# Kernel tuning notes

Measured on AMD Instinct MI355X. Metric: run time of the kernel, lower is better.

The kernel has to match this reference:

```python
import jax, jax.numpy as jnp
import numpy as np

K = 32  # knn neighborhood size (hard-coded in get_graph_feature)
EPS_BN = 1e-5


def _bn(x, g, b):
    # batch-norm (training-mode batch stats) over all axes except the last (channel) axis
    axes = tuple(range(x.ndim - 1))
    m = jnp.mean(x, axis=axes, keepdims=True)
    v = jnp.var(x, axis=axes, keepdims=True)
    return (x - m) * jax.lax.rsqrt(v + EPS_BN) * g + b


def _knn_idx(xt, k):
    # xt: [B, N, C] -> indices of k nearest points [B, N, k] (torch topk on -||xi-xj||^2)
    xx = jnp.sum(xt * xt, axis=-1)                       # [B, N]
    inner = jnp.einsum('bnc,bmc->bnm', xt, xt)           # [B, N, N]
    neg_d2 = -(xx[:, :, None] - 2.0 * inner + xx[:, None, :])
    _, idx = jax.lax.top_k(neg_d2, k)
    return idx


def _graph_feature(x, k=K):
    # x: [B, C, N] -> feature [B, N, k, 2C] matching torch cat((neighbors, center))
    xt = jnp.transpose(x, (0, 2, 1))                     # [B, N, C]
    idx = _knn_idx(xt, k)                                # [B, N, k]
    gathered = jax.vmap(lambda a, i: a[i])(xt, idx)      # [B, N, k, C]
    center = jnp.broadcast_to(xt[:, :, None, :], gathered.shape)
    return jnp.concatenate([gathered, center], axis=-1)


def _dgcnn(x, w1, w2, w3, w4, w5, g1, g2, g3, g4, g5, b1, b2, b3, b4, b5):
    # x: [B, 3, N] -> embeddings [B, emb, N]
    feat = _graph_feature(x)                                         # [B, N, K, 6]
    h = jax.nn.relu(_bn(jnp.einsum('bnkc,oc->bnko', feat, w1), g1, b1))
    x1 = jnp.max(h, axis=2)                                          # [B, N, 64]
    h = jax.nn.relu(_bn(jnp.einsum('bnkc,oc->bnko', h, w2), g2, b2))
    x2 = jnp.max(h, axis=2)
    h = jax.nn.relu(_bn(jnp.einsum('bnkc,oc->bnko', h, w3), g3, b3))
    x3 = jnp.max(h, axis=2)
    h = jax.nn.relu(_bn(jnp.einsum('bnkc,oc->bnko', h, w4), g4, b4))
    x4 = jnp.max(h, axis=2)
    cat = jnp.concatenate([x1, x2, x3, x4], axis=-1)                 # [B, N, 512]
    emb = jax.nn.relu(_bn(jnp.einsum('bnc,oc->bno', cat, w5), g5, b5))
    return jnp.transpose(emb, (0, 2, 1))                             # [B, emb, N]


def _pairwise_distance_batch(x, y):
    # x: [B, c, N], y: [B, c, M] -> euclidean distances [B, N, M] (faithful incl. clamp/mask)
    xx = jnp.sum(x * x, axis=1)                          # [B, N]
    yy = jnp.sum(y * y, axis=1)                          # [B, M]
    inner = jnp.einsum('bcn,bcm->bnm', x, y)
    pd = xx[:, :, None] - 2.0 * inner + yy[:, None, :]
    pd_sq = jnp.where(pd > 0.0, pd, 0.0)
    err = (pd_sq <= 0.0).astype(pd.dtype)
    d = jnp.sqrt(pd_sq + err * 1e-16)
    return d * (1.0 - err)


def setup_inputs() -> dict:
    key = jax.random.key(0)
    ks = jax.random.split(key, 20)
    B, N = 4, 2048
    def w(k, o, i):
        return jax.random.normal(k, (o, i), jnp.float32) * (1.0 / np.sqrt(i))
    inp = {
        'src': jax.random.normal(ks[0], (B, 3, N), jnp.float32),
        'tgt': jax.random.normal(ks[1], (B, 3, N), jnp.float32),
        'w1': w(ks[2], 64, 6), 'w2': w(ks[3], 64, 64), 'w3': w(ks[4], 128, 64),
        'w4': w(ks[5], 256, 128), 'w5': w(ks[6], 512, 512),
        'g1': jnp.ones(64), 'g2': jnp.ones(64), 'g3': jnp.ones(128),
        'g4': jnp.ones(256), 'g5': jnp.ones(512),
        'b1': jnp.zeros(64), 'b2': jnp.zeros(64), 'b3': jnp.zeros(128),
        'b4': jnp.zeros(256), 'b5': jnp.zeros(512),
    }
    return inp


def reference(src, tgt, w1, w2, w3, w4, w5, g1, g2, g3, g4, g5, b1, b2, b3, b4, b5):
    params = (w1, w2, w3, w4, w5, g1, g2, g3, g4, g5, b1, b2, b3, b4, b5)
    f_src = _dgcnn(src, *params)                         # [B, emb, N]
    f_tgt = _dgcnn(tgt, *params)                         # [B, emb, N] (siamese)
    d = _pairwise_distance_batch(f_src, f_tgt)           # [B, N, M]
    scores = jax.nn.softmax(-d, axis=-1)                 # soft correspondence
    src_corr = jnp.einsum('bcm,bnm->bcn', tgt, scores)   # tgt @ scores^T, [B, 3, N]
    return src_corr
```

## Files before the change

kernel.cpp:

```cpp
#include <hip/hip_runtime.h>
#include <hip/hip_bf16.h>
#include <math.h>

#define BB 4
#define NN 2048
#define KK 32
#define GG 2
constexpr int BNr = BB * NN;
constexpr int SGr = BB * NN * KK;
constexpr int SR  = GG * SGr;

typedef __hip_bfloat16 bf16;
typedef __attribute__((ext_vector_type(8))) short bf16x8;
typedef __attribute__((ext_vector_type(4))) short s16x4;
typedef __attribute__((ext_vector_type(4))) float f32x4;
__device__ __forceinline__ float b2f(bf16 v) { return __bfloat162float(v); }
__device__ __forceinline__ bf16  f2b(float v) { return __float2bfloat16(v); }
__device__ __forceinline__ short f2bs(float v) { bf16 b = f2b(v); return *(short*)&b; }
__device__ __forceinline__ float bs2f(short s) { bf16 b; *(short*)&b = s; return b2f(b); }

#define SWZ128(b) ((b) ^ ((((b) >> 7) & 7) << 4))
#define SWZ256(b) ((b) ^ ((((b) >> 8) & 7) << 4))

__global__ __launch_bounds__(256) void knn_kernel(const float* __restrict__ src,
                                                  const float* __restrict__ tgt,
                                                  int* __restrict__ idx_out,
                                                  float* __restrict__ g1part) {
    __shared__ float pts[3 * NN];
    __shared__ float xxs[NN];
    __shared__ int   sel[4][32];
    __shared__ float Gs[27];
    int blk = blockIdx.x;
    int gb = blk >> 9;
    int chunk = blk & 511;
    int g = gb >> 2, b = gb & 3;
    const float* x = (g == 0 ? src : tgt) + (size_t)b * 3 * NN;
    int t = threadIdx.x;
    if (t < 27) Gs[t] = 0.f;
    for (int i = t; i < 3 * NN; i += 256) pts[i] = x[i];
    __syncthreads();
    for (int m = t; m < NN; m += 256) {
        float p0 = pts[m], p1 = pts[NN + m], p2 = pts[2 * NN + m];
        xxs[m] = p0 * p0 + p1 * p1 + p2 * p2;
    }
    __syncthreads();
    int w = t >> 6, l = t & 63;
    int n = chunk * 4 + w;
    float q0 = pts[n], q1 = pts[NN + n], q2 = pts[2 * NN + n];
    float xxn = xxs[n];
    float d2[32];
#pragma unroll
    for (int s = 0; s < 32; ++s) {
        int m = s * 64 + l;
        float dot = q0 * pts[m] + q1 * pts[NN + m] + q2 * pts[2 * NN + m];
        d2[s] = (xxn - 2.0f * dot) + xxs[m];
    }
    float gval[4]; int gslot[4];
#pragma unroll
    for (int G = 0; G < 4; ++G) {
        float v = d2[G * 8]; int sl = G * 8;
#pragma unroll
        for (int s = 1; s < 8; ++s)
            if (d2[G * 8 + s] < v) { v = d2[G * 8 + s]; sl = G * 8 + s; }
        gval[G] = v; gslot[G] = sl;
    }
    int* outp = idx_out + ((size_t)gb * NN + n) * KK;
    for (int k = 0; k < KK; ++k) {
        float bv = fminf(fminf(gval[0], gval[1]), fminf(gval[2], gval[3]));
        float gv = bv;
#pragma unroll
        for (int off = 1; off < 64; off <<= 1) gv = fminf(gv, __shfl_xor(gv, off));
        unsigned long long mask = __ballot(bv == gv);
        int winner = (int)__builtin_ctzll(mask);
        if (l == winner) {
            int grp = (gval[0] == gv) ? 0 : (gval[1] == gv) ? 1 : (gval[2] == gv) ? 2 : 3;
#pragma unroll
            for (int G = 0; G < 4; ++G)
                if (G == grp) {
                    int bs = gslot[G];
                    outp[k] = bs * 64 + l;
                    sel[w][k] = bs * 64 + l;
#pragma unroll
                    for (int s = 0; s < 8; ++s)
                        if (G * 8 + s == bs) d2[G * 8 + s] = INFINITY;
                    float v = d2[G * 8]; int sl = G * 8;
#pragma unroll
                    for (int s = 1; s < 8; ++s)
                        if (d2[G * 8 + s] < v) { v = d2[G * 8 + s]; sl = G * 8 + s; }
                    gval[G] = v; gslot[G] = sl;
                }
        }
    }
    __syncthreads();
    float nx = 0.f, ny = 0.f, nz = 0.f;
    if (l < 32) {
        int m = sel[w][l];
        nx = pts[m]; ny = pts[NN + m]; nz = pts[2 * NN + m];
    }
    float v9[9] = {nx * nx, nx * ny, nx * nz, ny * ny, ny * nz, nz * nz, nx, ny, nz};
#pragma unroll
    for (int e = 0; e < 9; ++e) {
#pragma unroll
        for (int off = 1; off < 64; off <<= 1) v9[e] += __shfl_xor(v9[e], off);
    }
    if (l == 0) {
        float c3[3] = {q0, q1, q2};
#pragma unroll
        for (int e = 0; e < 6; ++e) atomicAdd(&Gs[e], v9[e]);
#pragma unroll
        for (int a = 0; a < 3; ++a)
#pragma unroll
            for (int bb = 0; bb < 3; ++bb)
                atomicAdd(&Gs[6 + a * 3 + bb], v9[6 + a] * c3[bb]);
        atomicAdd(&Gs[15], 32.f * q0 * q0);
        atomicAdd(&Gs[16], 32.f * q0 * q1);
        atomicAdd(&Gs[17], 32.f * q0 * q2);
        atomicAdd(&Gs[18], 32.f * q1 * q1);
        atomicAdd(&Gs[19], 32.f * q1 * q2);
        atomicAdd(&Gs[20], 32.f * q2 * q2);
        atomicAdd(&Gs[21], v9[6]);
        atomicAdd(&Gs[22], v9[7]);
        atomicAdd(&Gs[23], v9[8]);
        atomicAdd(&Gs[24], 32.f * q0);
        atomicAdd(&Gs[25], 32.f * q1);
        atomicAdd(&Gs[26], 32.f * q2);
    }
    __syncthreads();
    if (t < 27) g1part[(size_t)blk * 32 + t] = Gs[t];
}

__global__ __launch_bounds__(256) void reduce_g1_kernel(const float* __restrict__ part,
                                                        float* __restrict__ g1s) {
    __shared__ float red[256];
    int bx = blockIdx.x;
    int g = bx / 27, e = bx - g * 27;
    int t = threadIdx.x;
    float s = 0.f;
    for (int b = t; b < 2048; b += 256) s += part[((size_t)g * 2048 + b) * 32 + e];
    red[t] = s; __syncthreads();
    for (int st = 128; st > 0; st >>= 1) { if (t < st) red[t] += red[t + st]; __syncthreads(); }
    if (t == 0) g1s[g * 27 + e] = red[0];
}

__global__ void zero_kernel(float* __restrict__ p, int n) {
    int i = blockIdx.x * 256 + threadIdx.x;
    if (i < n) p[i] = 0.f;
}

__global__ void cvt_all_kernel(const float* __restrict__ w2, const float* __restrict__ w3,
                               const float* __restrict__ w4, const float* __restrict__ w5,
                               bf16* __restrict__ w2b, bf16* __restrict__ w3b,
                               bf16* __restrict__ w4b, bf16* __restrict__ w5b) {
    int i = blockIdx.x * 256 + threadIdx.x;
    if (i < 4096)   w2b[i] = f2b(w2[i]);
    if (i < 8192)   w3b[i] = f2b(w3[i]);
    if (i < 32768)  w4b[i] = f2b(w4[i]);
    if (i < 262144) w5b[i] = f2b(w5[i]);
}

__global__ void finalize_bn_kernel(float* __restrict__ sums, int C,
                                   const float* __restrict__ gamma,
                                   const float* __restrict__ beta,
                                   float cnt, float* __restrict__ params) {
    int i = blockIdx.x * blockDim.x + threadIdx.x;
    if (i >= GG * C) return;
    int g = i / C, c = i - g * C;
    float s  = sums[(g * 512 + c) * 2 + 0];
    float sq = sums[(g * 512 + c) * 2 + 1];
    float mean = s / cnt;
    float var = sq / cnt - mean * mean;
    if (var < 0.f) var = 0.f;
    float sc = gamma[c] * rsqrtf(var + 1e-5f);
    params[(g * 512 + c) * 2 + 0] = sc;
    params[(g * 512 + c) * 2 + 1] = beta[c] - mean * sc;
    sums[(g * 512 + c) * 2 + 0] = 0.f;
    sums[(g * 512 + c) * 2 + 1] = 0.f;
}

__global__ void finalize_l1_kernel(const float* __restrict__ g1s,
                                   const float* __restrict__ w1,
                                   const float* __restrict__ gamma,
                                   const float* __restrict__ beta,
                                   float cnt, float* __restrict__ params) {
    int i = blockIdx.x * blockDim.x + threadIdx.x;
    if (i >= GG * 64) return;
    int g = i >> 6, o = i & 63;
    const float* G = g1s + g * 27;
    float wv[6];
#pragma unroll
    for (int c = 0; c < 6; ++c) wv[c] = w1[o * 6 + c];
    float s = wv[0] * G[21] + wv[1] * G[22] + wv[2] * G[23] +
              wv[3] * G[24] + wv[4] * G[25] + wv[5] * G[26];
    const int UT[6][6] = {{0, 1, 2, 6, 7, 8},   {1, 3, 4, 9, 10, 11},
                          {2, 4, 5, 12, 13, 14},{6, 9, 12, 15, 16, 17},
                          {7, 10, 13, 16, 18, 19},{8, 11, 14, 17, 19, 20}};
    float q = 0.f;
#pragma unroll
    for (int a = 0; a < 6; ++a)
#pragma unroll
        for (int bb = 0; bb < 6; ++bb) q += wv[a] * wv[bb] * G[UT[a][bb]];
    float mean = s / cnt;
    float var = q / cnt - mean * mean;
    if (var < 0.f) var = 0.f;
    float sc = gamma[o] * rsqrtf(var + 1e-5f);
    params[(g * 512 + o) * 2 + 0] = sc;
    params[(g * 512 + o) * 2 + 1] = beta[o] - mean * sc;
}

__global__ __launch_bounds__(256, 3) void l12_mfma(
    const float* __restrict__ src, const float* __restrict__ tgt,
    const float* __restrict__ w1, const bf16* __restrict__ w2b,
    const int* __restrict__ idx, const float* __restrict__ p1,
    bf16* __restrict__ H2, bf16* __restrict__ cat, float* __restrict__ sums) {
    __shared__ char F1s[32768];
    __shared__ char W2s[8192];
    __shared__ float epiA[512];
    __shared__ float epiB[128];
    int tid = threadIdx.x;
    int w = tid >> 6, l = tid & 63, lg = l >> 4, lr = l & 15;
    long long row0 = (long long)blockIdx.x * 256;
    int g = (int)(row0 / SGr);

    epiA[tid] = 0.f; epiA[tid + 256] = 0.f;
    if (tid < 128) epiB[tid] = 0.f;
    for (int s = tid; s < 512; s += 256)
        *(bf16x8*)(W2s + SWZ128(s * 16)) = *(const bf16x8*)(w2b + s * 8);

    bf16x8 af[4];
#pragma unroll
    for (int i = 0; i < 4; ++i) {
        af[i] = (bf16x8){0, 0, 0, 0, 0, 0, 0, 0};
        if (lg == 0) {
            int rr = (int)row0 + w * 64 + 16 * i + lr;
            int nrow = rr >> 5;
            int n = nrow & (NN - 1);
            int gb = nrow >> 11;
            int b = gb & 3, gg = gb >> 2;
            const float* x = (gg ? tgt : src) + (size_t)b * 3 * NN;
            int j = idx[rr];
            af[i][0] = f2bs(x[j]);
            af[i][1] = f2bs(x[NN + j]);
            af[i][2] = f2bs(x[2 * NN + j]);
            af[i][3] = f2bs(x[n]);
            af[i][4] = f2bs(x[NN + n]);
            af[i][5] = f2bs(x[2 * NN + n]);
        }
    }
    bf16x8 bf1[4];
#pragma unroll
    for (int j = 0; j < 4; ++j) {
        bf1[j] = (bf16x8){0, 0, 0, 0, 0, 0, 0, 0};
        if (lg == 0) {
            int o = 16 * j + lr;
#pragma unroll
            for (int c = 0; c < 6; ++c) bf1[j][c] = f2bs(w1[o * 6 + c]);
        }
    }

    f32x4 acc1[4][4] = {};
#pragma unroll
    for (int i = 0; i < 4; ++i)
#pragma unroll
        for (int j = 0; j < 4; ++j)
            acc1[i][j] = __builtin_amdgcn_mfma_f32_16x16x32_bf16(af[i], bf1[j], acc1[i][j], 0, 0, 0);

    __syncthreads();

#pragma unroll
    for (int j = 0; j < 4; ++j) {
        int c = 16 * j + lr;
        float sc = p1[(g * 512 + c) * 2], sh = p1[(g * 512 + c) * 2 + 1];
#pragma unroll
        for (int i = 0; i < 4; ++i) {
            float m = 0.f;
#pragma unroll
            for (int r = 0; r < 4; ++r) {
                float v = fmaf(acc1[i][j][r], sc, sh);
                v = v > 0.f ? v : 0.f;
                m = fmaxf(m, v);
                int rowi = w * 64 + 16 * i + 4 * lg + r;
                *(bf16*)(F1s + SWZ128((rowi * 64 + c) * 2)) = f2b(v);
            }
            int p = 2 * w + (i >> 1);
            atomicMax((int*)epiA + p * 64 + c, __float_as_int(m));
        }
    }
    __syncthreads();

    {
        long long pt0 = row0 >> 5;
        for (int e = tid; e < 512; e += 256) {
            int p = e >> 6, c = e & 63;
            cat[(pt0 + p) * 512 + c] = f2b(__int_as_float(((int*)epiA)[p * 64 + c]));
        }
    }

    f32x4 acc2[4][4] = {};
#pragma unroll
    for (int ks = 0; ks < 2; ++ks) {
        bf16x8 bv[4];
#pragma unroll
        for (int j = 0; j < 4; ++j)
            bv[j] = *(bf16x8*)(W2s + SWZ128(((16 * j + lr) * 64 + ks * 32 + lg * 8) * 2));
#pragma unroll
        for (int i = 0; i < 4; ++i) {
            bf16x8 a = *(bf16x8*)(F1s + SWZ128(((w * 64 + 16 * i + lr) * 64 + ks * 32 + lg * 8) * 2));
#pragma unroll
            for (int j = 0; j < 4; ++j)
                acc2[i][j] = __builtin_amdgcn_mfma_f32_16x16x32_bf16(a, bv[j], acc2[i][j], 0, 0, 0);
        }
    }

#pragma unroll
    for (int j = 0; j < 4; ++j) {
        int c = 16 * j + lr;
        float s = 0.f, q = 0.f;
#pragma unroll
        for (int i = 0; i < 4; ++i)
#pragma unroll
            for (int r = 0; r < 4; ++r) {
                float v = acc2[i][j][r];
                s += v; q += v * v;
                long long gr = row0 + w * 64 + 16 * i + 4 * lg + r;
                H2[gr * 64 + c] = f2b(v);
            }
        s += __shfl_xor(s, 16); s += __shfl_xor(s, 32);
        q += __shfl_xor(q, 16); q += __shfl_xor(q, 32);
        if (lg == 0) {
            atomicAdd(&epiB[c * 2], s);
            atomicAdd(&epiB[c * 2 + 1], q);
        }
    }
    __syncthreads();
    if (tid < 128) atomicAdd(&sums[g * 1024 + tid], epiB[tid]);
}

template <int APPLY>
__global__ __launch_bounds__(512, 2) void chain34_mfma(
    const bf16* __restrict__ H2, const bf16* __restrict__ w3b,
    const bf16* __restrict__ w4b, const float* __restrict__ p2,
    const float* __restrict__ p3, const float* __restrict__ p4,
    bf16* __restrict__ cat, float* __restrict__ sums) {
    extern __shared__ char smem[];
    char* W3s = smem;
    char* A2s = smem + 16384;
    char* F3s = smem + 32768;
    float* P3s = (float*)(smem + 65536);
    float* P4s = (float*)(smem + 66560);
    float* epi = (float*)(smem + 68608);
    float* P2s = (float*)(smem + 72704);

    int tid = threadIdx.x;
    int w = tid >> 6, l = tid & 63, lg = l >> 4, lr = l & 15;
    long long rowB0 = (long long)blockIdx.x * 512;
    int g = (int)(rowB0 / SGr);

    for (int s = tid; s < 1024; s += 512)
        *(bf16x8*)(W3s + SWZ128(s * 16)) = *(const bf16x8*)(w3b + s * 8);
    if (tid < 256) P3s[tid] = p3[g * 1024 + tid];
    if (tid < 128) P2s[tid] = p2[g * 1024 + tid];
    P4s[tid] = p4 ? p4[g * 1024 + tid] : 0.f;

    bf16x8 rv0 = *(const bf16x8*)(H2 + rowB0 * 64 + (long long)tid * 8);
    bf16x8 rv1 = *(const bf16x8*)(H2 + rowB0 * 64 + (long long)(tid + 512) * 8);
    __syncthreads();

    float sc3[4], sh3[4];
#pragma unroll
    for (int r = 0; r < 4; ++r) {
        int c = 16 * w + 4 * lg + r;
        sc3[r] = P3s[c * 2]; sh3[r] = P3s[c * 2 + 1];
    }
    float sc4[2][4], sh4[2][4];
    if (APPLY) {
#pragma unroll
        for (int i = 0; i < 2; ++i)
#pragma unroll
            for (int r = 0; r < 4; ++r) {
                int c = 16 * (2 * w + i) + 4 * lg + r;
                sc4[i][r] = P4s[c * 2]; sh4[i][r] = P4s[c * 2 + 1];
            }
    }
    float sacc[2][4] = {}, qacc[2][4] = {};

    auto bn2w = [&](bf16x8 rv, int s) {
        int cb = (s & 7) * 8;
        bf16x8 ov;
#pragma unroll
        for (int e = 0; e < 8; ++e) {
            float v = fmaf(bs2f(rv[e]), P2s[(cb + e) * 2], P2s[(cb + e) * 2 + 1]);
            v = v > 0.f ? v : 0.f;
            ov[e] = f2bs(v);
        }
        *(bf16x8*)(A2s + SWZ128(s * 16)) = ov;
    };
    bn2w(rv0, tid); bn2w(rv1, tid + 512);
    __syncthreads();

    for (int chunk = 0; chunk < 4; ++chunk) {
        long long row0 = rowB0 + chunk * 128;
        {
            f32x4 acc3[8] = {};
#pragma unroll
            for (int ks = 0; ks < 2; ++ks) {
                bf16x8 wf = *(bf16x8*)(W3s + SWZ128(((16 * w + lr) * 64 + ks * 32 + lg * 8) * 2));
#pragma unroll
                for (int j = 0; j < 8; ++j) {
                    bf16x8 a2 = *(bf16x8*)(A2s + SWZ128(((16 * j + lr) * 64 + ks * 32 + lg * 8) * 2));
                    acc3[j] = __builtin_amdgcn_mfma_f32_16x16x32_bf16(wf, a2, acc3[j], 0, 0, 0);
                }
            }
#pragma unroll
            for (int j = 0; j < 8; ++j) {
                s16x4 pk;
#pragma unroll
                for (int r = 0; r < 4; ++r) {
                    float v = fmaf(acc3[j][r], sc3[r], sh3[r]);
                    v = v > 0.f ? v : 0.f;
                    pk[r] = f2bs(v);
                }
                *(s16x4*)(F3s + SWZ256(((16 * j + lr) * 128 + 16 * w + 4 * lg) * 2)) = pk;
            }
        }
        if (chunk < 3) {
            long long rn = rowB0 + (chunk + 1) * 128;
            rv0 = *(const bf16x8*)(H2 + rn * 64 + (long long)tid * 8);
            rv1 = *(const bf16x8*)(H2 + rn * 64 + (long long)(tid + 512) * 8);
        }
        __syncthreads();

        f32x4 acc4[2][8] = {};
#pragma unroll
        for (int ks = 0; ks < 4; ++ks) {
            bf16x8 a0 = *(const bf16x8*)(w4b + (16 * (2 * w) + lr) * 128 + ks * 32 + lg * 8);
            bf16x8 a1 = *(const bf16x8*)(w4b + (16 * (2 * w + 1) + lr) * 128 + ks * 32 + lg * 8);
#pragma unroll
            for (int j = 0; j < 8; ++j) {
                bf16x8 bfr = *(bf16x8*)(F3s + SWZ256(((16 * j + lr) * 128 + ks * 32 + lg * 8) * 2));
                acc4[0][j] = __builtin_amdgcn_mfma_f32_16x16x32_bf16(a0, bfr, acc4[0][j], 0, 0, 0);
                acc4[1][j] = __builtin_amdgcn_mfma_f32_16x16x32_bf16(a1, bfr, acc4[1][j], 0, 0, 0);
            }
        }

        if (!APPLY) {
#pragma unroll
            for (int i = 0; i < 2; ++i)
#pragma unroll
                for (int r = 0; r < 4; ++r) {
                    float s = 0.f, q = 0.f;
#pragma unroll
                    for (int j = 0; j < 8; ++j) {
                        float v = acc4[i][j][r];
                        s += v; q += v * v;
                    }
                    sacc[i][r] += s; qacc[i][r] += q;
                }
        } else {
#pragma unroll
            for (int i = 0; i < 2; ++i)
#pragma unroll
                for (int r = 0; r < 4; ++r) {
                    float sc = sc4[i][r], sh = sh4[i][r];
#pragma unroll
                    for (int p = 0; p < 4; ++p) {
                        float v0 = fmaf(acc4[i][2 * p][r], sc, sh);
                        float v1 = fmaf(acc4[i][2 * p + 1][r], sc, sh);
                        v0 = v0 > 0.f ? v0 : 0.f;
                        v1 = v1 > 0.f ? v1 : 0.f;
                        float m = fmaxf(v0, v1);
                        m = fmaxf(m, __shfl_xor(m, 1));
                        m = fmaxf(m, __shfl_xor(m, 2));
                        m = fmaxf(m, __shfl_xor(m, 4));
                        m = fmaxf(m, __shfl_xor(m, 8));
                        if (lr == 0)
                            epi[p * 256 + 16 * (2 * w + i) + 4 * lg + r] = m;
                    }
                }
            __syncthreads();
            long long pt0 = row0 >> 5;
            for (int e = tid; e < 1024; e += 512) {
                int p = e >> 8, c = e & 255;
                cat[(pt0 + p) * 512 + 256 + c] = f2b(epi[e]);
            }
            {
                int p = tid >> 7, c = tid & 127;
                float m = 0.f;
                for (int r = 0; r < 32; ++r)
                    m = fmaxf(m, b2f(*(bf16*)(F3s + SWZ256(((p * 32 + r) * 128 + c) * 2))));
                cat[(pt0 + p) * 512 + 128 + c] = f2b(m);
            }
        }
        __syncthreads();
        if (chunk < 3) {
            bn2w(rv0, tid); bn2w(rv1, tid + 512);
            __syncthreads();
        }
    }
    if (!APPLY) {
#pragma unroll
        for (int i = 0; i < 2; ++i)
#pragma unroll
            for (int r = 0; r < 4; ++r) {
                float s = sacc[i][r], q = qacc[i][r];
                s += __shfl_xor(s, 1); s += __shfl_xor(s, 2);
                s += __shfl_xor(s, 4); s += __shfl_xor(s, 8);
                q += __shfl_xor(q, 1); q += __shfl_xor(q, 2);
                q += __shfl_xor(q, 4); q += __shfl_xor(q, 8);
                if (lr == 0) {
                    int c = 16 * (2 * w + i) + 4 * lg + r;
                    atomicAdd(&sums[g * 1024 + c * 2], s);
                    atomicAdd(&sums[g * 1024 + c * 2 + 1], q);
                }
            }
    }
}

template <int MODE, int CH, int BNA>
__global__ __launch_bounds__(256, 4) void mfma_gemm(
    const bf16* __restrict__ A, const bf16* __restrict__ Wt,
    float* __restrict__ OutF, bf16* __restrict__ OutB,
    int Cin, int ldOut, long long sA, long long sW, long long sO,
    int rowsPerGroup, const float* __restrict__ params, float* __restrict__ sums,
    const float* __restrict__ pba, bf16* __restrict__ cat) {
    __shared__ char As[16384];
    __shared__ char Bs[8192];
    __shared__ float epi[128];
    __shared__ float PBs[128];
    __shared__ int x2m[256];
    int tid = threadIdx.x;
    int w = tid >> 6, l = tid & 63, lg = l >> 4, lr = l & 15;
    int bz = blockIdx.z;
    const bf16* Ap = A + (long long)bz * sA;
    const bf16* Wp = Wt + (long long)bz * sW;
    int o0 = blockIdx.y * 64;
    long long rowB0 = (long long)blockIdx.x * (128 * CH);
    int g = (int)(rowB0 / rowsPerGroup);
    if ((MODE == 1 || MODE == 3) && tid < 128) epi[tid] = 0.f;
    if (BNA && tid < 128) PBs[tid] = pba[g * 1024 + tid];
    int wr = (w >> 1) * 64, wc = (w & 1) * 32;

    for (int ch = 0; ch < CH; ++ch) {
        long long row0 = rowB0 + (long long)ch * 128;
        if (BNA) {
            __syncthreads();
            if (tid < 256) x2m[tid] = 0;
        }
        f32x4 acc[4][2] = {};
        for (int k0 = 0; k0 < Cin; k0 += 64) {
            __syncthreads();
            for (int s = tid; s < 1024; s += 256) {
                if (BNA) {
                    bf16x8 rv = *(const bf16x8*)(Ap + (row0 + (s >> 3)) * Cin + k0 + (s & 7) * 8);
                    int cb = k0 + (s & 7) * 8;
                    int pt = (s >> 3) >> 5;
                    bf16x8 ov;
#pragma unroll
                    for (int e = 0; e < 8; ++e) {
                        float v = fmaf(bs2f(rv[e]), PBs[(cb + e) * 2], PBs[(cb + e) * 2 + 1]);
                        v = v > 0.f ? v : 0.f;
                        ov[e] = f2bs(v);
                        atomicMax(&x2m[pt * 64 + cb + e], __float_as_int(v));
                    }
                    *(bf16x8*)(As + SWZ128(s * 16)) = ov;
                } else {
                    *(bf16x8*)(As + SWZ128(s * 16)) =
                        *(const bf16x8*)(Ap + (row0 + (s >> 3)) * Cin + k0 + (s & 7) * 8);
                }
            }
            for (int s = tid; s < 512; s += 256)
                *(bf16x8*)(Bs + SWZ128(s * 16)) =
                    *(const bf16x8*)(Wp + (long long)(o0 + (s >> 3)) * Cin + k0 + (s & 7) * 8);
            __syncthreads();
#pragma unroll
            for (int ks = 0; ks < 2; ++ks) {
                bf16x8 b0 = *(bf16x8*)(Bs + SWZ128(((wc + lr) * 64 + ks * 32 + lg * 8) * 2));
                bf16x8 b1 = *(bf16x8*)(Bs + SWZ128(((wc + 16 + lr) * 64 + ks * 32 + lg * 8) * 2));
#pragma unroll
                for (int i = 0; i < 4; ++i) {
                    bf16x8 a = *(bf16x8*)(As + SWZ128(((wr + 16 * i + lr) * 64 + ks * 32 + lg * 8) * 2));
                    acc[i][0] = __builtin_amdgcn_mfma_f32_16x16x32_bf16(a, b0, acc[i][0], 0, 0, 0);
                    acc[i][1] = __builtin_amdgcn_mfma_f32_16x16x32_bf16(a, b1, acc[i][1], 0, 0, 0);
                }
            }
        }
        if (BNA && blockIdx.y == 0) {
            long long pt0 = row0 >> 5;
            if (tid < 256) {
                int p = tid >> 6, c = tid & 63;
                cat[(pt0 + p) * 512 + 64 + c] = f2b(__int_as_float(x2m[tid]));
            }
        }
        if (MODE == 1 || MODE == 3) {
#pragma unroll
            for (int j = 0; j < 2; ++j) {
                int c = wc + 16 * j + lr;
                float s = 0.f, q = 0.f;
#pragma unroll
                for (int i = 0; i < 4; ++i)
#pragma unroll
                    for (int r = 0; r < 4; ++r) {
                        float v = acc[i][j][r];
                        s += v; q += v * v;
                    }
                s += __shfl_xor(s, 16); s += __shfl_xor(s, 32);
                q += __shfl_xor(q, 16); q += __shfl_xor(q, 32);
                if (lg == 0) {
                    atomicAdd(&epi[c * 2], s);
                    atomicAdd(&epi[c * 2 + 1], q);
                }
            }
        }
        if (MODE == 0 || MODE == 3) {
            float* Op = OutF + (long long)bz * sO;
#pragma unroll
            for (int j = 0; j < 2; ++j) {
                int gc = o0 + wc + 16 * j + lr;
#pragma unroll
                for (int i = 0; i < 4; ++i)
#pragma unroll
                    for (int r = 0; r < 4; ++r) {
                        long long gr = row0 + wr + 16 * i + 4 * lg + r;
                        Op[gr * ldOut + gc] = acc[i][j][r];
                    }
            }
        }
    }
    if (MODE == 1 || MODE == 3) {
        __syncthreads();
        if (tid < 128) atomicAdd(&sums[g * 1024 + o0 * 2 + tid], epi[tid]);
    }
}

__global__ __launch_bounds__(256) void emb_finalize(const float* __restrict__ h5,
                                                    const float* __restrict__ p5,
                                                    bf16* __restrict__ embB,
                                                    float* __restrict__ nrm) {
    __shared__ float red[256];
    int row = blockIdx.x; int t = threadIdx.x;
    int g = row / BNr;
    float s = 0.f;
#pragma unroll
    for (int i = 0; i < 2; ++i) {
        int c = t + i * 256;
        float v = fmaf(h5[(size_t)row * 512 + c], p5[(g * 512 + c) * 2], p5[(g * 512 + c) * 2 + 1]);
        v = v > 0.f ? v : 0.f;
        bf16 bb = f2b(v);
        embB[(size_t)row * 512 + c] = bb;
        float vb = b2f(bb);
        s += vb * vb;
    }
    red[t] = s; __syncthreads();
    for (int st = 128; st > 0; st >>= 1) { if (t < st) red[t] += red[t + st]; __syncthreads(); }
    if (t == 0) nrm[row] = red[0];
}

__global__ __launch_bounds__(256) void corr_kernel(const float* __restrict__ inner,
                                                   const float* __restrict__ nrm,
                                                   const float* __restrict__ tgt,
                                                   float* __restrict__ out) {
    __shared__ float red[256];
    int blk = blockIdx.x;
    int b = blk >> 11, n = blk & (NN - 1);
    int t = threadIdx.x;
    const float* inr = inner + ((size_t)b * NN + n) * NN;
    float xx = nrm[b * NN + n];
    float dloc[8];
    float vmax = -INFINITY;
#pragma unroll
    for (int i = 0; i < 8; ++i) {
        int m = t + i * 256;
        float pd = (xx - 2.f * inr[m]) + nrm[BNr + b * NN + m];
        float d = pd > 0.f ? sqrtf(pd) : 0.f;
        dloc[i] = d;
        vmax = fmaxf(vmax, -d);
    }
    red[t] = vmax; __syncthreads();
    for (int s = 128; s > 0; s >>= 1) { if (t < s) red[t] = fmaxf(red[t], red[t + s]); __syncthreads(); }
    vmax = red[0]; __syncthreads();
    const float* tp = tgt + (size_t)b * 3 * NN;
    float se = 0.f, s0 = 0.f, s1 = 0.f, s2 = 0.f;
#pragma unroll
    for (int i = 0; i < 8; ++i) {
        int m = t + i * 256;
        float p = expf(-dloc[i] - vmax);
        se += p;
        s0 += p * tp[m]; s1 += p * tp[NN + m]; s2 += p * tp[2 * NN + m];
    }
    red[t] = se; __syncthreads();
    for (int s = 128; s > 0; s >>= 1) { if (t < s) red[t] += red[t + s]; __syncthreads(); }
    float tot = red[0]; __syncthreads();
    red[t] = s0; __syncthreads();
    for (int s = 128; s > 0; s >>= 1) { if (t < s) red[t] += red[t + s]; __syncthreads(); }
    float o0v = red[0]; __syncthreads();
    red[t] = s1; __syncthreads();
    for (int s = 128; s > 0; s >>= 1) { if (t < s) red[t] += red[t + s]; __syncthreads(); }
    float o1v = red[0]; __syncthreads();
    red[t] = s2; __syncthreads();
    for (int s = 128; s > 0; s >>= 1) { if (t < s) red[t] += red[t + s]; __syncthreads(); }
    float o2v = red[0];
    if (t == 0) {
        out[(size_t)b * 3 * NN + n]          = o0v / tot;
        out[(size_t)b * 3 * NN + NN + n]     = o1v / tot;
        out[(size_t)b * 3 * NN + 2 * NN + n] = o2v / tot;
    }
}

extern "C" void kernel_launch(void* const* d_in, const int* in_sizes, int n_in,
                              void* d_out, int out_size, void* d_ws, size_t ws_size,
                              hipStream_t stream) {
    const float* src = (const float*)d_in[0];
    const float* tgt = (const float*)d_in[1];
    const float* w1  = (const float*)d_in[2];
    const float* w2  = (const float*)d_in[3];
    const float* w3  = (const float*)d_in[4];
    const float* w4  = (const float*)d_in[5];
    const float* w5  = (const float*)d_in[6];
    const float* g1  = (const float*)d_in[7];
    const float* g2  = (const float*)d_in[8];
    const float* g3  = (const float*)d_in[9];
    const float* g4  = (const float*)d_in[10];
    const float* g5  = (const float*)d_in[11];
    const float* b1  = (const float*)d_in[12];
    const float* b2  = (const float*)d_in[13];
    const float* b3  = (const float*)d_in[14];
    const float* b4  = (const float*)d_in[15];
    const float* b5  = (const float*)d_in[16];
    float* out = (float*)d_out;
    char* ws = (char*)d_ws;
    (void)in_sizes; (void)n_in;

    size_t off = 0;
    auto alloc = [&](size_t bytes) { size_t o = off; off = (off + bytes + 255) & ~(size_t)255; return o; };
    int*   idx    = (int*)(ws + alloc((size_t)SR * 4));
    bf16*  H2     = (bf16*)(ws + alloc((size_t)SR * 64 * 2));
    bf16*  cat    = (bf16*)(ws + alloc((size_t)GG * BNr * 512 * 2));
    bf16*  embB   = (bf16*)(ws + alloc((size_t)GG * BNr * 512 * 2));
    float* h5     = (float*)(ws + alloc((size_t)GG * BNr * 512 * 4));
    float* nrm    = (float*)(ws + alloc((size_t)GG * BNr * 4));
    float* sums   = (float*)(ws + alloc(2048 * 4));
    float* g1s    = (float*)(ws + alloc(64 * 4));
    float* g1part = (float*)(ws + alloc((size_t)GG * 2048 * 32 * 4));
    float* prm    = (float*)(ws + alloc(5 * 2048 * 4));
    bf16*  w2b    = (bf16*)(ws + alloc(4096 * 2));
    bf16*  w3b    = (bf16*)(ws + alloc(8192 * 2));
    bf16*  w4b    = (bf16*)(ws + alloc(32768 * 2));
    bf16*  w5b    = (bf16*)(ws + alloc(262144 * 2));
    float* P1 = prm, *P2 = prm + 2048, *P3 = prm + 4096, *P4 = prm + 6144, *P5 = prm + 8192;
    float* inner = (float*)H2;

    if (ws_size < off) {
        hipMemsetAsync(d_out, 0, (size_t)out_size * 4, stream);
        return;
    }

    zero_kernel<<<8, 256, 0, stream>>>(sums, 2048);
    knn_kernel<<<GG * BB * NN / 4, 256, 0, stream>>>(src, tgt, idx, g1part);
    cvt_all_kernel<<<1024, 256, 0, stream>>>(w2, w3, w4, w5, w2b, w3b, w4b, w5b);

    reduce_g1_kernel<<<GG * 27, 256, 0, stream>>>(g1part, g1s);
    finalize_l1_kernel<<<1, 128, 0, stream>>>(g1s, w1, g1, b1, (float)SGr, P1);

    l12_mfma<<<SR / 256, 256, 0, stream>>>(src, tgt, w1, w2b, idx, P1, H2, cat, sums);
    finalize_bn_kernel<<<1, 128, 0, stream>>>(sums, 64, g2, b2, (float)SGr, P2);

    mfma_gemm<1, 4, 1><<<dim3(SR / 512, 2, 1), 256, 0, stream>>>(
        H2, w3b, nullptr, nullptr, 64, 0, 0, 0, 0, SGr, nullptr, sums, P2, cat);
    finalize_bn_kernel<<<2, 128, 0, stream>>>(sums, 128, g3, b3, (float)SGr, P3);

    chain34_mfma<0><<<1024, 512, 73216, stream>>>(H2, w3b, w4b, P2, P3, nullptr, nullptr, sums);
    finalize_bn_kernel<<<4, 128, 0, stream>>>(sums, 256, g4, b4, (float)SGr, P4);
    chain34_mfma<1><<<1024, 512, 73216, stream>>>(H2, w3b, w4b, P2, P3, P4, cat, nullptr);

    mfma_gemm<3, 1, 0><<<dim3(GG * BNr / 128, 8, 1), 256, 0, stream>>>(
        cat, w5b, h5, nullptr, 512, 512, 0, 0, 0, BNr, nullptr, sums, nullptr, nullptr);
    finalize_bn_kernel<<<8, 128, 0, stream>>>(sums, 512, g5, b5, (float)BNr, P5);
    emb_finalize<<<GG * BNr, 256, 0, stream>>>(h5, P5, embB, nrm);

    mfma_gemm<0, 1, 0><<<dim3(NN / 128, NN / 64, BB), 256, 0, stream>>>(
        embB, embB + (size_t)BNr * 512, inner, nullptr, 512, 2048,
        (long long)NN * 512, (long long)NN * 512, (long long)NN * NN,
        SGr, nullptr, nullptr, nullptr, nullptr);

    corr_kernel<<<BB * NN, 256, 0, stream>>>(inner, nrm, tgt, out);
}
```

Baseline: 719.9 us.

## Stage W4 in LDS and swap MFMA operand roles in chain34 layer-4 GEMM

```diff
diff --git a/kernel.cpp b/kernel.cpp
--- a/kernel.cpp
+++ b/kernel.cpp
@@ -343,12 +343,13 @@
     bf16* __restrict__ cat, float* __restrict__ sums) {
     extern __shared__ char smem[];
     char* W3s = smem;
-    char* A2s = smem + 16384;
-    char* F3s = smem + 32768;
-    float* P3s = (float*)(smem + 65536);
-    float* P4s = (float*)(smem + 66560);
-    float* epi = (float*)(smem + 68608);
-    float* P2s = (float*)(smem + 72704);
+    char* W4s = smem + 16384;
+    char* A2s = smem + 81920;
+    char* F3s = smem + 98304;
+    float* P3s = (float*)(smem + 131072);
+    float* P4s = (float*)(smem + 132096);
+    float* epi = (float*)(smem + 134144);
+    float* P2s = (float*)(smem + 138240);
 
     int tid = threadIdx.x;
     int w = tid >> 6, l = tid & 63, lg = l >> 4, lr = l & 15;
@@ -357,12 +358,12 @@
 
     for (int s = tid; s < 1024; s += 512)
         *(bf16x8*)(W3s + SWZ128(s * 16)) = *(const bf16x8*)(w3b + s * 8);
+    for (int s = tid; s < 4096; s += 512)
+        *(bf16x8*)(W4s + SWZ256(s * 16)) = *(const bf16x8*)(w4b + s * 8);
     if (tid < 256) P3s[tid] = p3[g * 1024 + tid];
     if (tid < 128) P2s[tid] = p2[g * 1024 + tid];
     P4s[tid] = p4 ? p4[g * 1024 + tid] : 0.f;
-
-    bf16x8 rv0 = *(const bf16x8*)(H2 + rowB0 * 64 + (long long)tid * 8);
-    bf16x8 rv1 = *(const bf16x8*)(H2 + rowB0 * 64 + (long long)(tid + 512) * 8);
+    if (!APPLY) epi[tid] = 0.f;
     __syncthreads();
 
     float sc3[4], sh3[4];
@@ -371,34 +372,24 @@
         int c = 16 * w + 4 * lg + r;
         sc3[r] = P3s[c * 2]; sh3[r] = P3s[c * 2 + 1];
     }
-    float sc4[2][4], sh4[2][4];
-    if (APPLY) {
-#pragma unroll
-        for (int i = 0; i < 2; ++i)
-#pragma unroll
-            for (int r = 0; r < 4; ++r) {
-                int c = 16 * (2 * w + i) + 4 * lg + r;
-                sc4[i][r] = P4s[c * 2]; sh4[i][r] = P4s[c * 2 + 1];
-            }
-    }
-    float sacc[2][4] = {}, qacc[2][4] = {};
-
-    auto bn2w = [&](bf16x8 rv, int s) {
-        int cb = (s & 7) * 8;
-        bf16x8 ov;
-#pragma unroll
-        for (int e = 0; e < 8; ++e) {
-            float v = fmaf(bs2f(rv[e]), P2s[(cb + e) * 2], P2s[(cb + e) * 2 + 1]);
-            v = v > 0.f ? v : 0.f;
-            ov[e] = f2bs(v);
-        }
-        *(bf16x8*)(A2s + SWZ128(s * 16)) = ov;
-    };
-    bn2w(rv0, tid); bn2w(rv1, tid + 512);
-    __syncthreads();
 
     for (int chunk = 0; chunk < 4; ++chunk) {
         long long row0 = rowB0 + chunk * 128;
+        for (int s = tid; s < 1024; s += 512) {
+            bf16x8 rv = *(const bf16x8*)(H2 + row0 * 64 + s * 8);
+            int cb = (s & 7) * 8;
+            bf16x8 ov;
+#pragma unroll
+            for (int e = 0; e < 8; ++e) {
+                float v = fmaf(bs2f(rv[e]), P2s[(cb + e) * 2], P2s[(cb + e) * 2 + 1]);
+                v = v > 0.f ? v : 0.f;
+                ov[e] = f2bs(v);
+            }
+            *(bf16x8*)(A2s + SWZ128(s * 16)) = ov;
+        }
+        if (APPLY) { ((int*)epi)[tid] = 0; ((int*)epi)[tid + 512] = 0; }
+        __syncthreads();
+
         {
             f32x4 acc3[8] = {};
 #pragma unroll
@@ -422,65 +413,55 @@
                 *(s16x4*)(F3s + SWZ256(((16 * j + lr) * 128 + 16 * w + 4 * lg) * 2)) = pk;
             }
         }
-        if (chunk < 3) {
-            long long rn = rowB0 + (chunk + 1) * 128;
-            rv0 = *(const bf16x8*)(H2 + rn * 64 + (long long)tid * 8);
-            rv1 = *(const bf16x8*)(H2 + rn * 64 + (long long)(tid + 512) * 8);
-        }
         __syncthreads();
 
-        f32x4 acc4[2][8] = {};
+        f32x4 acc4[16] = {};
 #pragma unroll
         for (int ks = 0; ks < 4; ++ks) {
-            bf16x8 a0 = *(const bf16x8*)(w4b + (16 * (2 * w) + lr) * 128 + ks * 32 + lg * 8);
-            bf16x8 a1 = *(const bf16x8*)(w4b + (16 * (2 * w + 1) + lr) * 128 + ks * 32 + lg * 8);
-#pragma unroll
-            for (int j = 0; j < 8; ++j) {
-                bf16x8 bfr = *(bf16x8*)(F3s + SWZ256(((16 * j + lr) * 128 + ks * 32 + lg * 8) * 2));
-                acc4[0][j] = __builtin_amdgcn_mfma_f32_16x16x32_bf16(a0, bfr, acc4[0][j], 0, 0, 0);
-                acc4[1][j] = __builtin_amdgcn_mfma_f32_16x16x32_bf16(a1, bfr, acc4[1][j], 0, 0, 0);
+            bf16x8 a = *(bf16x8*)(F3s + SWZ256(((16 * w + lr) * 128 + ks * 32 + lg * 8) * 2));
+#pragma unroll
+            for (int j = 0; j < 16; ++j) {
+                bf16x8 b = *(bf16x8*)(W4s + SWZ256(((16 * j + lr) * 128 + ks * 32 + lg * 8) * 2));
+                acc4[j] = __builtin_amdgcn_mfma_f32_16x16x32_bf16(a, b, acc4[j], 0, 0, 0);
             }
         }
 
         if (!APPLY) {
 #pragma unroll
-            for (int i = 0; i < 2; ++i)
+            for (int j = 0; j < 16; ++j) {
+                int c = 16 * j + lr;
+                float s = acc4[j][0] + acc4[j][1] + acc4[j][2] + acc4[j][3];
+                float q = acc4[j][0] * acc4[j][0] + acc4[j][1] * acc4[j][1] +
+                          acc4[j][2] * acc4[j][2] + acc4[j][3] * acc4[j][3];
+                s += __shfl_xor(s, 16); s += __shfl_xor(s, 32);
+                q += __shfl_xor(q, 16); q += __shfl_xor(q, 32);
+                if (lg == 0) {
+                    atomicAdd(&epi[c * 2], s);
+                    atomicAdd(&epi[c * 2 + 1], q);
+                }
+            }
+        } else {
+#pragma unroll
+            for (int j = 0; j < 16; ++j) {
+                int c = 16 * j + lr;
+                float sc = P4s[c * 2], sh = P4s[c * 2 + 1];
+                float m = 0.f;
 #pragma unroll
                 for (int r = 0; r < 4; ++r) {
-                    float s = 0.f, q = 0.f;
-#pragma unroll
-                    for (int j = 0; j < 8; ++j) {
-                        float v = acc4[i][j][r];
-                        s += v; q += v * v;
-                    }
-                    sacc[i][r] += s; qacc[i][r] += q;
+                    float v = fmaf(acc4[j][r], sc, sh);
+                    v = v > 0.f ? v : 0.f;
+                    m = fmaxf(m, v);
                 }
-        } else {
-#pragma unroll
-            for (int i = 0; i < 2; ++i)
-#pragma unroll
-                for (int r = 0; r < 4; ++r) {
-                    float sc = sc4[i][r], sh = sh4[i][r];
-#pragma unroll
-                    for (int p = 0; p < 4; ++p) {
-                        float v0 = fmaf(acc4[i][2 * p][r], sc, sh);
-                        float v1 = fmaf(acc4[i][2 * p + 1][r], sc, sh);
-                        v0 = v0 > 0.f ? v0 : 0.f;
-                        v1 = v1 > 0.f ? v1 : 0.f;
-                        float m = fmaxf(v0, v1);
-                        m = fmaxf(m, __shfl_xor(m, 1));
-                        m = fmaxf(m, __shfl_xor(m, 2));
-                        m = fmaxf(m, __shfl_xor(m, 4));
-                        m = fmaxf(m, __shfl_xor(m, 8));
-                        if (lr == 0)
-                            epi[p * 256 + 16 * (2 * w + i) + 4 * lg + r] = m;
-                    }
-                }
+                m = fmaxf(m, __shfl_xor(m, 16));
+                m = fmaxf(m, __shfl_xor(m, 32));
+                if (lg == 0)
+                    atomicMax((int*)epi + (w >> 1) * 256 + c, __float_as_int(m));
+            }
             __syncthreads();
             long long pt0 = row0 >> 5;
             for (int e = tid; e < 1024; e += 512) {
                 int p = e >> 8, c = e & 255;
-                cat[(pt0 + p) * 512 + 256 + c] = f2b(epi[e]);
+                cat[(pt0 + p) * 512 + 256 + c] = f2b(__int_as_float(((int*)epi)[p * 256 + c]));
             }
             {
                 int p = tid >> 7, c = tid & 127;
@@ -491,27 +472,9 @@
             }
         }
         __syncthreads();
-        if (chunk < 3) {
-            bn2w(rv0, tid); bn2w(rv1, tid + 512);
-            __syncthreads();
-        }
     }
     if (!APPLY) {
-#pragma unroll
-        for (int i = 0; i < 2; ++i)
-#pragma unroll
-            for (int r = 0; r < 4; ++r) {
-                float s = sacc[i][r], q = qacc[i][r];
-                s += __shfl_xor(s, 1); s += __shfl_xor(s, 2);
-                s += __shfl_xor(s, 4); s += __shfl_xor(s, 8);
-                q += __shfl_xor(q, 1); q += __shfl_xor(q, 2);
-                q += __shfl_xor(q, 4); q += __shfl_xor(q, 8);
-                if (lr == 0) {
-                    int c = 16 * (2 * w + i) + 4 * lg + r;
-                    atomicAdd(&sums[g * 1024 + c * 2], s);
-                    atomicAdd(&sums[g * 1024 + c * 2 + 1], q);
-                }
-            }
+        atomicAdd(&sums[g * 1024 + tid], epi[tid]);
     }
 }
 
@@ -767,9 +730,9 @@
         H2, w3b, nullptr, nullptr, 64, 0, 0, 0, 0, SGr, nullptr, sums, P2, cat);
     finalize_bn_kernel<<<2, 128, 0, stream>>>(sums, 128, g3, b3, (float)SGr, P3);
 
-    chain34_mfma<0><<<1024, 512, 73216, stream>>>(H2, w3b, w4b, P2, P3, nullptr, nullptr, sums);
+    chain34_mfma<0><<<1024, 512, 138752, stream>>>(H2, w3b, w4b, P2, P3, nullptr, nullptr, sums);
     finalize_bn_kernel<<<4, 128, 0, stream>>>(sums, 256, g4, b4, (float)SGr, P4);
-    chain34_mfma<1><<<1024, 512, 73216, stream>>>(H2, w3b, w4b, P2, P3, P4, cat, nullptr);
+    chain34_mfma<1><<<1024, 512, 138752, stream>>>(H2, w3b, w4b, P2, P3, P4, cat, nullptr);
 
     mfma_gemm<3, 1, 0><<<dim3(GG * BNr / 128, 8, 1), 256, 0, stream>>>(
         cat, w5b, h5, nullptr, 512, 512, 0, 0, 0, BNr, nullptr, sums, nullptr, nullptr);
```

Measured after the change: 673.4 us. -6.5%, faster.
